# Kernel tuning notes

Hardware: AMD Instinct MI355X
Metric: run time of the kernel (lower is better)

Reference implementation:

```python
import jax, jax.numpy as jnp
import numpy as np

B, N, K = 8, 2048, 8
NEG_SLOPE = 0.2
EPS = 1e-5


def lrelu(x):
    return jax.nn.leaky_relu(x, NEG_SLOPE)


def bn(x, axes):
    # BatchNorm forward with batch statistics, affine at init (gamma=1, beta=0)
    m = x.mean(axes, keepdims=True)
    v = x.var(axes, keepdims=True)
    return (x - m) / jnp.sqrt(v + EPS)


def knn(x, k):
    # x: [B, C, N] -> idx [B, N, K] of nearest neighbors (incl. self), as in DGCNN
    xx = jnp.sum(x * x, axis=1)                      # [B, N]
    inner = jnp.einsum('bcn,bcm->bnm', x, x)         # [B, N, N]
    pair = -(xx[:, :, None] - 2.0 * inner + xx[:, None, :])  # -||xi-xj||^2
    return jax.lax.top_k(pair, k)[1]                 # [B, N, K]


def get_graph_feature(x, idx):
    # x: [B, C, N], idx: [B, N, K] -> [B, 2C, N, K] = cat(neighbor-center, center)
    nb = jax.vmap(lambda xb, ib: xb[:, ib])(x, idx)  # [B, C, N, K]
    ctr = x[:, :, :, None]
    return jnp.concatenate([nb - ctr, jnp.broadcast_to(ctr, nb.shape)], axis=1)


def edge_block(e, W):
    # 1x1 conv2d (no bias) + BN2d + LeakyReLU on [B, C, N, K]
    h = jnp.einsum('oc,bcnk->bonk', W, e)
    return lrelu(bn(h, (0, 2, 3)))


def setup_inputs() -> dict:
    key = jax.random.key(0)
    ks = jax.random.split(key, 10)
    def w(k, shape):
        fan_in = shape[-1]
        return jax.random.normal(k, shape, jnp.float32) / np.sqrt(fan_in)
    return {
        'x': jax.random.normal(ks[0], (B, N, 3), jnp.float32),
        'start_neighs': jax.random.randint(ks[1], (B, N, K), 0, N, jnp.int32),
        'u_noise': jax.random.uniform(ks[2], (B, 70, N), jnp.float32, 1e-6, 1.0 - 1e-6),
        'W0': w(ks[3], (64, 6)),
        'W1': w(ks[4], (128, 128)),
        'W2': w(ks[5], (256, 256)),
        'W3': w(ks[6], (512, 512)),
        'W4': w(ks[7], (1024, 960)),
        'Wm1': w(ks[8], (512, 1024)),
        'Wm2': w(ks[9], (70, 512)),
    }


def reference(x, start_neighs, u_noise, W0, W1, W2, W3, W4, Wm1, Wm2):
    xt = jnp.swapaxes(x, 1, 2)                        # [B, 3, N]
    # EdgeConv 0: uses provided start_neighs
    e = get_graph_feature(xt, start_neighs)           # [B, 6, N, K]
    h = edge_block(e, W0)                             # [B, 64, N, K]
    outs = [h.max(axis=-1)]                           # [B, 64, N]
    # EdgeConvs 1..3: dynamic knn on current features (only_true_neighs=False)
    for W in (W1, W2, W3):
        prev = outs[-1]
        idx = knn(prev, K)
        e = get_graph_feature(prev, idx)              # [B, 2C, N, K]
        h = edge_block(e, W)
        outs.append(h.max(axis=-1))
    cat = jnp.concatenate(outs, axis=1)               # [B, 960, N]
    feat = lrelu(bn(jnp.einsum('oc,bcn->bon', W4, cat), (0, 2)))  # [B, 1024, N]
    # masking prediction head
    hm = lrelu(bn(jnp.einsum('oc,bcn->bon', Wm1, feat), (0, 2)))  # [B, 512, N]
    logits = jnp.einsum('oc,bcn->bon', Wm2, hm)       # [B, 70, N]
    # gumbel softmax (tau=1, hard=True) over last dim (points), straight-through
    g = -jnp.log(-jnp.log(u_noise))
    soft = jax.nn.softmax(logits + g, axis=-1)
    hard = jax.nn.one_hot(jnp.argmax(soft, axis=-1), N, dtype=soft.dtype)
    y = hard + soft - jax.lax.stop_gradient(soft)     # values are exactly 0/1
    return jnp.transpose(y, (1, 0, 2))[..., None]     # [70, B, N, 1]
```

## Files before the change

### kernel.cpp

```cpp
#include <hip/hip_runtime.h>
#include <math.h>

#define Bsz 8
#define Nsz 2048
#define Ksz 8
#define NSLOPE 0.2f
#define EPSV 1e-5f
#define LOSCALE 2048.0f
#define INV_LOSCALE (1.0f / 2048.0f)

typedef _Float16 half8 __attribute__((ext_vector_type(8)));
typedef float floatx4 __attribute__((ext_vector_type(4)));

__device__ __forceinline__ int swzk(int k, int row)
{
    return (k & ~31) | ((((k >> 3) + (row >> 1)) & 3) << 3) | (k & 7);
}

__device__ __forceinline__ void glds16(const _Float16* g, _Float16* l)
{
    __builtin_amdgcn_global_load_lds(
        (const __attribute__((address_space(1))) unsigned int*)g,
        (__attribute__((address_space(3))) unsigned int*)l, 16, 0, 0);
}

__device__ __forceinline__ void split2(float v, _Float16& h, _Float16& l)
{
    _Float16 hh = (_Float16)v;
    h = hh;
    l = (_Float16)((v - (float)hh) * LOSCALE);
}

__device__ __forceinline__ unsigned long long shfl_xor64(unsigned long long x, int off)
{
    unsigned lo = __shfl_xor((unsigned)x, off, 64);
    unsigned hi = __shfl_xor((unsigned)(x >> 32), off, 64);
    return ((unsigned long long)hi << 32) | lo;
}

__device__ __forceinline__ void ins8_64(unsigned long long (&t)[8], unsigned long long key)
{
#pragma unroll
    for (int j = 7; j >= 1; --j)
        t[j] = (key > t[j - 1]) ? t[j - 1] : ((key > t[j]) ? key : t[j]);
    t[0] = (key > t[0]) ? key : t[0];
}

template <int EPI>
__launch_bounds__(512) __global__
void hgemm_k(const _Float16* __restrict__ Ahi, const _Float16* __restrict__ Alo,
             long long sAb, int lda,
             const _Float16* __restrict__ Bhi, const _Float16* __restrict__ Blo,
             long long sBb, int ldb,
             float* __restrict__ C, long long sCb, int ldc,
             int Mreal, int Kk, const float* __restrict__ xx)
{
    __shared__ _Float16 sm[16384];
    const int b = blockIdx.z;
    const int m0 = blockIdx.y * 128, n0 = blockIdx.x * 128;
    const int tid = threadIdx.x;
    const int w = tid >> 6, lane = tid & 63;
    const int quad = lane >> 4, r16 = lane & 15;
    const int wm = (w >> 1) * 32, wn = (w & 1) * 64;
    const int sq = (r16 >> 1) & 3;
    const int kchunk = ((quad + sq) & 3) * 8;

    const _Float16* Ah = Ahi + (long long)b * sAb;
    const _Float16* Al = Alo + (long long)b * sAb;
    const _Float16* Bh = Bhi + (long long)b * sBb;
    const _Float16* Bl = Blo + (long long)b * sBb;

    floatx4 acc_h[2][4], acc_m[2][4];
#pragma unroll
    for (int i = 0; i < 2; i++)
#pragma unroll
        for (int j = 0; j < 4; j++) {
            acc_h[i][j] = (floatx4){0.f, 0.f, 0.f, 0.f};
            acc_m[i][j] = (floatx4){0.f, 0.f, 0.f, 0.f};
        }

    const int srow = tid >> 2;
    const int sseg = (tid & 3) * 8;

    for (int k0 = 0; k0 < Kk; k0 += 32) {
        long long aoff = (long long)(m0 + srow) * lda + k0 + sseg;
        long long boff = (long long)(n0 + srow) * ldb + k0 + sseg;
        glds16(Ah + aoff, &sm[tid * 8]);
        glds16(Al + aoff, &sm[4096 + tid * 8]);
        glds16(Bh + boff, &sm[8192 + tid * 8]);
        glds16(Bl + boff, &sm[12288 + tid * 8]);
        __syncthreads();

        half8 ah[2], al[2];
#pragma unroll
        for (int i = 0; i < 2; i++) {
            int off = (wm + i * 16 + r16) * 32 + kchunk;
            ah[i] = *(const half8*)&sm[off];
            al[i] = *(const half8*)&sm[4096 + off];
        }
#pragma unroll
        for (int j = 0; j < 4; j++) {
            int off = (wn + j * 16 + r16) * 32 + kchunk;
            half8 bh = *(const half8*)&sm[8192 + off];
            half8 bl = *(const half8*)&sm[12288 + off];
#pragma unroll
            for (int i = 0; i < 2; i++) {
                acc_h[i][j] = __builtin_amdgcn_mfma_f32_16x16x32_f16(ah[i], bh, acc_h[i][j], 0, 0, 0);
                acc_m[i][j] = __builtin_amdgcn_mfma_f32_16x16x32_f16(ah[i], bl, acc_m[i][j], 0, 0, 0);
                acc_m[i][j] = __builtin_amdgcn_mfma_f32_16x16x32_f16(al[i], bh, acc_m[i][j], 0, 0, 0);
            }
        }
        __syncthreads();
    }

    float* Cb = C + (long long)b * sCb;
    const float* xxp = EPI ? (xx + (long long)b * Nsz) : xx;
#pragma unroll
    for (int i = 0; i < 2; i++) {
#pragma unroll
        for (int r = 0; r < 4; r++) {
            int gm = m0 + wm + i * 16 + quad * 4 + r;
            if (gm >= Mreal) continue;
            float xm = EPI ? xxp[gm] : 0.f;
#pragma unroll
            for (int j = 0; j < 4; j++) {
                int gn = n0 + wn + j * 16 + r16;
                float v = acc_h[i][j][r] + acc_m[i][j][r] * INV_LOSCALE;
                if (EPI == 1) v = -((xm - 2.f * v) + xxp[gn]);
                Cb[(long long)gm * ldc + gn] = v;
            }
        }
    }
}

__launch_bounds__(512) __global__
void hgemm_cand_k(const _Float16* __restrict__ Phi, const _Float16* __restrict__ Plo,
                  long long sPb, int ldp,
                  unsigned long long* __restrict__ cand,
                  int Kk, const float* __restrict__ xx)
{
    __shared__ float smf[64 * 129];
    _Float16* sm = (_Float16*)smf;
    const int b = blockIdx.z;
    const int m0 = blockIdx.y * 128, n0 = blockIdx.x * 128;
    const int tid = threadIdx.x;
    const int w = tid >> 6, lane = tid & 63;
    const int quad = lane >> 4, r16 = lane & 15;
    const int wm = (w >> 1) * 32, wn = (w & 1) * 64;
    const int sq = (r16 >> 1) & 3;
    const int kchunk = ((quad + sq) & 3) * 8;

    const _Float16* Ah = Phi + (long long)b * sPb;
    const _Float16* Al = Plo + (long long)b * sPb;

    floatx4 acc_h[2][4], acc_m[2][4];
#pragma unroll
    for (int i = 0; i < 2; i++)
#pragma unroll
        for (int j = 0; j < 4; j++) {
            acc_h[i][j] = (floatx4){0.f, 0.f, 0.f, 0.f};
            acc_m[i][j] = (floatx4){0.f, 0.f, 0.f, 0.f};
        }

    const int srow = tid >> 2;
    const int sseg = (tid & 3) * 8;

    for (int k0 = 0; k0 < Kk; k0 += 32) {
        long long aoff = (long long)(m0 + srow) * ldp + k0 + sseg;
        long long boff = (long long)(n0 + srow) * ldp + k0 + sseg;
        glds16(Ah + aoff, &sm[tid * 8]);
        glds16(Al + aoff, &sm[4096 + tid * 8]);
        glds16(Ah + boff, &sm[8192 + tid * 8]);
        glds16(Al + boff, &sm[12288 + tid * 8]);
        __syncthreads();

        half8 ah[2], al[2];
#pragma unroll
        for (int i = 0; i < 2; i++) {
            int off = (wm + i * 16 + r16) * 32 + kchunk;
            ah[i] = *(const half8*)&sm[off];
            al[i] = *(const half8*)&sm[4096 + off];
        }
#pragma unroll
        for (int j = 0; j < 4; j++) {
            int off = (wn + j * 16 + r16) * 32 + kchunk;
            half8 bh = *(const half8*)&sm[8192 + off];
            half8 bl = *(const half8*)&sm[12288 + off];
#pragma unroll
            for (int i = 0; i < 2; i++) {
                acc_h[i][j] = __builtin_amdgcn_mfma_f32_16x16x32_f16(ah[i], bh, acc_h[i][j], 0, 0, 0);
                acc_m[i][j] = __builtin_amdgcn_mfma_f32_16x16x32_f16(ah[i], bl, acc_m[i][j], 0, 0, 0);
                acc_m[i][j] = __builtin_amdgcn_mfma_f32_16x16x32_f16(al[i], bh, acc_m[i][j], 0, 0, 0);
            }
        }
        __syncthreads();
    }

    const float* xxp = xx + (long long)b * Nsz;
    const int row8 = tid >> 3;
    const int s8 = tid & 7;
    const int gshift = (lane >> 3) * 8;

#pragma unroll
    for (int p = 0; p < 2; p++) {
        __syncthreads();
        if ((w >> 2) == p) {
            int rbase = wm - p * 64;
#pragma unroll
            for (int i = 0; i < 2; i++) {
#pragma unroll
                for (int r = 0; r < 4; r++) {
                    int row_l = rbase + i * 16 + quad * 4 + r;
                    float xm = xxp[m0 + p * 64 + row_l];
#pragma unroll
                    for (int j = 0; j < 4; j++) {
                        int col = wn + j * 16 + r16;
                        float a = acc_h[i][j][r] + acc_m[i][j][r] * INV_LOSCALE;
                        smf[row_l * 129 + col] = -((xm - 2.f * a) + xxp[n0 + col]);
                    }
                }
            }
        }
        __syncthreads();

        unsigned vals[16];
#pragma unroll
        for (int c = 0; c < 16; c++) {
            unsigned u = __float_as_uint(smf[row8 * 129 + s8 + c * 8]);
            vals[c] = (u & 0x80000000u) ? ~u : (u | 0x80000000u);
        }
        unsigned t[8] = {0, 0, 0, 0, 0, 0, 0, 0};
#pragma unroll
        for (int c = 0; c < 16; c++) {
            unsigned key = vals[c];
#pragma unroll
            for (int j = 7; j >= 1; --j) {
                unsigned m = t[j - 1] < key ? t[j - 1] : key;
                t[j] = t[j] > m ? t[j] : m;
            }
            t[0] = t[0] > key ? t[0] : key;
        }
#pragma unroll
        for (int d = 1; d < 8; d <<= 1) {
            unsigned oth[8];
#pragma unroll
            for (int j = 0; j < 8; j++) oth[j] = __shfl_xor(t[j], d, 64);
            unsigned c2[8];
#pragma unroll
            for (int j = 0; j < 8; j++) {
                unsigned a = t[j], b2 = oth[7 - j];
                c2[j] = a > b2 ? a : b2;
            }
#define CE(A, B) { unsigned x = c2[A], y = c2[B]; c2[A] = x > y ? x : y; c2[B] = x > y ? y : x; }
            CE(0, 4) CE(1, 5) CE(2, 6) CE(3, 7)
            CE(0, 2) CE(1, 3) CE(4, 6) CE(5, 7)
            CE(0, 1) CE(2, 3) CE(4, 5) CE(6, 7)
#undef CE
#pragma unroll
            for (int j = 0; j < 8; j++) t[j] = c2[j];
        }
        const unsigned T = t[7];

        int gm = m0 + p * 64 + row8;
        unsigned long long* cp = cand + (((size_t)b * Nsz + gm) * 16 + blockIdx.x) * 8;
        const unsigned smask = (1u << s8) - 1u;
        int g = 0;
#pragma unroll
        for (int c = 0; c < 16; c++) {
            unsigned long long m = __ballot(vals[c] > T);
            unsigned byte = (unsigned)(m >> gshift) & 0xFFu;
            if (vals[c] > T) {
                int pos = g + __popc(byte & smask);
                int gn = n0 + s8 + c * 8;
                cp[pos] = ((unsigned long long)vals[c] << 32) | (0xFFFFFFFFu - (unsigned)gn);
            }
            g += __popc(byte);
        }
        const int needed = 8 - g;
        int e = 0;
        for (int c = 0; c < 16 && e < needed; c++) {
            unsigned long long m = __ballot(vals[c] == T);
            unsigned byte = (unsigned)(m >> gshift) & 0xFFu;
            int pos = e + __popc(byte & smask);
            if (vals[c] == T && pos < needed) {
                int gn = n0 + s8 + c * 8;
                cp[g + pos] = ((unsigned long long)T << 32) | (0xFFFFFFFFu - (unsigned)gn);
            }
            e += __popc(byte);
        }
    }
}

__global__ void merge_cand_k(const unsigned long long* __restrict__ cand,
                             int* __restrict__ idxo)
{
    int lane = threadIdx.x & 63;
    int row = blockIdx.x * 4 + (threadIdx.x >> 6);
    const unsigned long long* cr = cand + (size_t)row * 128;
    unsigned long long t[8] = {0, 0, 0, 0, 0, 0, 0, 0};
    ins8_64(t, cr[lane]);
    ins8_64(t, cr[lane + 64]);
    int* op = idxo + (size_t)row * 8;
#pragma unroll
    for (int r = 0; r < 8; r++) {
        unsigned long long best = t[0];
#pragma unroll
        for (int off = 32; off; off >>= 1) {
            unsigned long long o = shfl_xor64(best, off);
            if (o > best) best = o;
        }
        bool own = (t[0] == best);
#pragma unroll
        for (int j = 0; j < 7; j++) t[j] = own ? t[j + 1] : t[j];
        t[7] = own ? 0ull : t[7];
        if (lane == 0) op[r] = (int)(0xFFFFFFFFu - (unsigned)(best & 0xFFFFFFFFull));
    }
}

__launch_bounds__(256) __global__
void sgemm_k(const float* __restrict__ A, int lda,
             const float* __restrict__ Bm, long long sBb, int ldb,
             float* __restrict__ C, long long sCb, int ldc,
             int M, int Kk)
{
    __shared__ float As[16][64];
    __shared__ float Bs[16][64];
    const int b = blockIdx.z;
    const float* Bb = Bm + (long long)b * sBb;
    const int m0 = blockIdx.y * 64, n0 = blockIdx.x * 64;
    const int tid = threadIdx.x;
    const int am = tid >> 2, ak = (tid & 3) * 4;
    const int bk = tid >> 6, bn = tid & 63;
    const int tx = tid & 15, ty = tid >> 4;
    float acc[4][4] = {};
    for (int k0 = 0; k0 < Kk; k0 += 16) {
#pragma unroll
        for (int i = 0; i < 4; i++) {
            int gk = k0 + ak + i;
            int gm = m0 + am;
            As[ak + i][am] = (gk < Kk && gm < M) ? A[(long long)gm * lda + gk] : 0.f;
        }
#pragma unroll
        for (int i = 0; i < 4; i++) {
            int kk = bk + i * 4;
            int gk = k0 + kk;
            Bs[kk][bn] = (gk < Kk) ? Bb[(long long)gk * ldb + (n0 + bn)] : 0.f;
        }
        __syncthreads();
#pragma unroll
        for (int kk = 0; kk < 16; kk++) {
            float a[4], bb2[4];
#pragma unroll
            for (int i = 0; i < 4; i++) a[i] = As[kk][ty * 4 + i];
#pragma unroll
            for (int j = 0; j < 4; j++) bb2[j] = Bs[kk][tx * 4 + j];
#pragma unroll
            for (int i = 0; i < 4; i++)
#pragma unroll
                for (int j = 0; j < 4; j++)
                    acc[i][j] = fmaf(a[i], bb2[j], acc[i][j]);
        }
        __syncthreads();
    }
    float* Cb = C + (long long)b * sCb;
#pragma unroll
    for (int i = 0; i < 4; i++) {
        int gm = m0 + ty * 4 + i;
        if (gm >= M) continue;
#pragma unroll
        for (int j = 0; j < 4; j++)
            Cb[(long long)gm * ldc + n0 + tx * 4 + j] = acc[i][j];
    }
}

#define T0 16384
#define T1 (T0 + 192)
#define T2 (T1 + 16384)
#define T3 (T2 + 65536)
#define T4 (T3 + 262144)
#define T5 (T4 + 983040)
#define T6 (T5 + 524288)
#define T7 (T6 + 65536)
#define WOFF_E1 0
#define WOFF_E2 16384
#define WOFF_E3 81920
#define WOFF_W4 344064
#define WOFF_M1 1327104
#define WOFF_M2 1851392

__device__ __forceinline__ void split_plain(const float* W, _Float16* wh, _Float16* wl,
                                            size_t base, int t, int M, int Kk)
{
    int oo = t / Kk, c = t - oo * Kk;
    float v = (oo < M) ? W[(size_t)oo * Kk + c] : 0.f;
    _Float16 h, l;
    split2(v, h, l);
    size_t d = base + (size_t)oo * Kk + swzk(c, oo);
    wh[d] = h; wl[d] = l;
}

__device__ __forceinline__ void split_edge(const float* W, _Float16* wh, _Float16* wl,
                                           size_t base, int t, int O, int C)
{
    int oo = t / C, c = t - oo * C;
    float v;
    if (oo < O) v = W[(size_t)oo * 2 * C + c];
    else { int o2 = oo - O; v = W[(size_t)o2 * 2 * C + C + c] - W[(size_t)o2 * 2 * C + c]; }
    _Float16 h, l;
    split2(v, h, l);
    size_t d = base + (size_t)oo * C + swzk(c, oo);
    wh[d] = h; wl[d] = l;
}

__global__ void mega_prep_k(const float* __restrict__ x,
                            const float* __restrict__ W0, const float* __restrict__ W1,
                            const float* __restrict__ W2, const float* __restrict__ W3,
                            const float* __restrict__ W4, const float* __restrict__ Wm1,
                            const float* __restrict__ Wm2,
                            float* __restrict__ xt, float* __restrict__ wcat32,
                            _Float16* __restrict__ wh, _Float16* __restrict__ wl)
{
    int t = blockIdx.x * 256 + threadIdx.x;
    if (t < T0) {
        int n = t & (Nsz - 1), b = t >> 11;
#pragma unroll
        for (int c = 0; c < 3; c++)
            xt[((size_t)b * 3 + c) * Nsz + n] = x[((size_t)b * Nsz + n) * 3 + c];
    } else if (t < T1) {
        int u = t - T0;
        int oo = u / 3, c = u % 3;
        float a = W0[(size_t)oo * 6 + c];
        float b2 = W0[(size_t)oo * 6 + 3 + c];
        wcat32[(size_t)oo * 3 + c] = a;
        wcat32[(size_t)(64 + oo) * 3 + c] = b2 - a;
    } else if (t < T2) {
        split_edge(W1, wh, wl, WOFF_E1, t - T1, 128, 64);
    } else if (t < T3) {
        split_edge(W2, wh, wl, WOFF_E2, t - T2, 256, 128);
    } else if (t < T4) {
        split_edge(W3, wh, wl, WOFF_E3, t - T3, 512, 256);
    } else if (t < T5) {
        split_plain(W4, wh, wl, WOFF_W4, t - T4, 1024, 960);
    } else if (t < T6) {
        split_plain(Wm1, wh, wl, WOFF_M1, t - T5, 512, 1024);
    } else if (t < T7) {
        split_plain(Wm2, wh, wl, WOFF_M2, t - T6, 70, 512);
    }
}

__global__ void xx_planes_k(const _Float16* __restrict__ catA, const _Float16* __restrict__ catB,
                            float* __restrict__ xx, int off, int C)
{
    int t = blockIdx.x * 256 + threadIdx.x;
    if (t >= Bsz * Nsz) return;
    int n = t & (Nsz - 1), b = t >> 11;
    size_t base = ((size_t)b * Nsz + n) * 1024 + off;
    float s = 0.f;
    for (int c8 = 0; c8 < C / 8; c8++) {
        half8 h = *(const half8*)&catA[base + c8 * 8];
        half8 l = *(const half8*)&catB[base + c8 * 8];
#pragma unroll
        for (int e = 0; e < 8; e++) {
            float vh = (float)h[e];
            float vl = (float)l[e] * INV_LOSCALE;
            s = fmaf(vh, vh, s);
            s = fmaf(2.f * vh, vl, s);
        }
    }
    xx[t] = s;
}

__global__ void gather_pool_t_k(const float* __restrict__ R, const int* __restrict__ idx,
                                _Float16* __restrict__ catA, _Float16* __restrict__ catB,
                                float* __restrict__ part, int O, int off)
{
    __shared__ float tile[64][65];
    const int tid = threadIdx.x;
    const int lane = tid & 63, w = tid >> 6;
    const int n0 = blockIdx.x * 64, o0 = blockIdx.y * 64, b = blockIdx.z;
    const int n = n0 + lane;

    int id[8];
    {
        const int* ip = idx + ((size_t)b * Nsz + n) * 8;
#pragma unroll
        for (int k = 0; k < 8; k++) id[k] = ip[k];
    }
    const float* Rb = R + (size_t)b * 2 * O * Nsz;
#pragma unroll
    for (int i = 0; i < 16; i++) {
        int o_l = w + i * 4;
        int o = o0 + o_l;
        const float* P = Rb + (size_t)o * Nsz;
        float q = Rb[(size_t)(O + o) * Nsz + n];
        float hmax = -INFINITY, s1 = 0.f, s2 = 0.f;
#pragma unroll
        for (int k = 0; k < 8; k++) {
            float h = P[id[k]] + q;
            hmax = fmaxf(hmax, h);
            s1 += h;
            s2 += h * h;
        }
        tile[o_l][lane] = hmax;
#pragma unroll
        for (int offs = 32; offs; offs >>= 1) {
            s1 += __shfl_xor(s1, offs, 64);
            s2 += __shfl_xor(s2, offs, 64);
        }
        if (lane == 0) {
            size_t pi = ((size_t)o * Bsz + b) * 32 + blockIdx.x;
            part[pi * 2] = s1;
            part[pi * 2 + 1] = s2;
        }
    }
    __syncthreads();
    int n_l = tid >> 2, quad = tid & 3;
    int nrow = n0 + n_l;
    half8 h0, h1, l0, l1;
#pragma unroll
    for (int e = 0; e < 8; e++) {
        _Float16 hh, ll;
        split2(tile[quad * 16 + e][n_l], hh, ll);
        h0[e] = hh; l0[e] = ll;
        split2(tile[quad * 16 + 8 + e][n_l], hh, ll);
        h1[e] = hh; l1[e] = ll;
    }
    size_t rowb = ((size_t)b * Nsz + nrow) * 1024;
    int c0 = off + o0 + quad * 16;
    *(half8*)&catA[rowb + swzk(c0, nrow)] = h0;
    *(half8*)&catA[rowb + swzk(c0 + 8, nrow)] = h1;
    *(half8*)&catB[rowb + swzk(c0, nrow)] = l0;
    *(half8*)&catB[rowb + swzk(c0 + 8, nrow)] = l1;
}

__global__ void stats_reduce_k(const float* __restrict__ part, float* __restrict__ stats)
{
    int o2 = blockIdx.x;
    int t = threadIdx.x;
    float s1 = part[((size_t)o2 * 256 + t) * 2];
    float s2 = part[((size_t)o2 * 256 + t) * 2 + 1];
#pragma unroll
    for (int off = 32; off; off >>= 1) { s1 += __shfl_xor(s1, off, 64); s2 += __shfl_xor(s2, off, 64); }
    __shared__ float sh[8];
    int w = t >> 6;
    if ((t & 63) == 0) { sh[w] = s1; sh[4 + w] = s2; }
    __syncthreads();
    if (t == 0) {
        stats[2 * o2] = sh[0] + sh[1] + sh[2] + sh[3];
        stats[2 * o2 + 1] = sh[4] + sh[5] + sh[6] + sh[7];
    }
}

__global__ void fc_stats_k(const float* __restrict__ buf, float* __restrict__ stats, int O)
{
    int oo = blockIdx.x;
    int t = threadIdx.x;
    float s1 = 0.f, s2 = 0.f;
    for (int i = t; i < Bsz * Nsz; i += 256) {
        int b = i >> 11, n = i & (Nsz - 1);
        float v = buf[((size_t)b * O + oo) * Nsz + n];
        s1 += v; s2 += v * v;
    }
#pragma unroll
    for (int off = 32; off; off >>= 1) { s1 += __shfl_xor(s1, off, 64); s2 += __shfl_xor(s2, off, 64); }
    __shared__ float sh[8];
    int w = t >> 6;
    if ((t & 63) == 0) { sh[w] = s1; sh[4 + w] = s2; }
    __syncthreads();
    if (t == 0) {
        stats[2 * oo] = sh[0] + sh[1] + sh[2] + sh[3];
        stats[2 * oo + 1] = sh[4] + sh[5] + sh[6] + sh[7];
    }
}

__global__ void bn_t_k(_Float16* __restrict__ catA, _Float16* __restrict__ catB,
                       const float* __restrict__ stats, int off, int O, float invCnt)
{
    int per_n = O / 8;
    size_t t = (size_t)blockIdx.x * 256 + threadIdx.x;
    if (t >= (size_t)Bsz * Nsz * per_n) return;
    int c8 = (int)(t % per_n);
    size_t rest = t / per_n;
    int n = (int)(rest & (Nsz - 1));
    int b = (int)(rest >> 11);
    size_t base = ((size_t)b * Nsz + n) * 1024 + off + c8 * 8;
    int oo_base = ((c8 >> 2) << 5) + ((((c8 & 3) - (n >> 1)) & 3) << 3);
    half8 h = *(const half8*)&catA[base];
    half8 l = *(const half8*)&catB[base];
    half8 ho, lo;
#pragma unroll
    for (int e = 0; e < 8; e++) {
        int oo = oo_base + e;
        float mean = stats[2 * oo] * invCnt;
        float var = stats[2 * oo + 1] * invCnt - mean * mean;
        float v = (float)h[e] + (float)l[e] * INV_LOSCALE;
        float z = (v - mean) / sqrtf(var + EPSV);
        z = z >= 0.f ? z : NSLOPE * z;
        _Float16 hh, ll;
        split2(z, hh, ll);
        ho[e] = hh; lo[e] = ll;
    }
    *(half8*)&catA[base] = ho;
    *(half8*)&catB[base] = lo;
}

__global__ void bn_split_t_k(const float* __restrict__ src, const float* __restrict__ stats,
                             _Float16* __restrict__ dA, _Float16* __restrict__ dB,
                             int O, int ldt, float invCnt)
{
    __shared__ float tile[64][65];
    const int tid = threadIdx.x;
    const int n0 = blockIdx.x * 64, o0 = blockIdx.y * 64, b = blockIdx.z;
#pragma unroll
    for (int i = 0; i < 16; i++) {
        int flat = tid + 256 * i;
        int o_l = flat >> 6, n_l = flat & 63;
        int oo = o0 + o_l;
        float mean = stats[2 * oo] * invCnt;
        float var = stats[2 * oo + 1] * invCnt - mean * mean;
        float v = src[((size_t)b * O + oo) * Nsz + n0 + n_l];
        float z = (v - mean) / sqrtf(var + EPSV);
        tile[o_l][n_l] = z >= 0.f ? z : NSLOPE * z;
    }
    __syncthreads();
    int n_l = tid >> 2, quad = tid & 3;
    int nrow = n0 + n_l;
    half8 h0, h1, l0, l1;
#pragma unroll
    for (int e = 0; e < 8; e++) {
        _Float16 hh, ll;
        split2(tile[quad * 16 + e][n_l], hh, ll);
        h0[e] = hh; l0[e] = ll;
        split2(tile[quad * 16 + 8 + e][n_l], hh, ll);
        h1[e] = hh; l1[e] = ll;
    }
    size_t rowb = ((size_t)b * Nsz + nrow) * ldt;
    int c0 = o0 + quad * 16;
    *(half8*)&dA[rowb + swzk(c0, nrow)] = h0;
    *(half8*)&dA[rowb + swzk(c0 + 8, nrow)] = h1;
    *(half8*)&dB[rowb + swzk(c0, nrow)] = l0;
    *(half8*)&dB[rowb + swzk(c0 + 8, nrow)] = l1;
}

__global__ void gumbel_onehot_k(const float* __restrict__ logits, const float* __restrict__ u,
                                float* __restrict__ out)
{
    int lane = threadIdx.x & 63;
    int wv = threadIdx.x >> 6;
    int row = blockIdx.x * 4 + wv;
    int b = row / 70, oo = row % 70;
    const float* L = logits + (size_t)row * Nsz;
    const float* U = u + (size_t)row * Nsz;
    float bv = -INFINITY; int bi = 0x7fffffff;
    for (int n = lane; n < Nsz; n += 64) {
        float g = -logf(-logf(U[n]));
        float z = L[n] + g;
        if (z > bv) { bv = z; bi = n; }
    }
#pragma unroll
    for (int off = 32; off; off >>= 1) {
        float ov = __shfl_xor(bv, off, 64);
        int oi = __shfl_xor(bi, off, 64);
        if (ov > bv || (ov == bv && oi < bi)) { bv = ov; bi = oi; }
    }
    float* Or = out + ((size_t)oo * Bsz + b) * Nsz;
    for (int n = lane; n < Nsz; n += 64) Or[n] = (n == bi) ? 1.f : 0.f;
}

extern "C" void kernel_launch(void* const* d_in, const int* in_sizes, int n_in,
                              void* d_out, int out_size, void* d_ws, size_t ws_size,
                              hipStream_t stream)
{
    (void)in_sizes; (void)n_in; (void)out_size; (void)ws_size;
    const float* x   = (const float*)d_in[0];
    const int*   sn  = (const int*)d_in[1];
    const float* un  = (const float*)d_in[2];
    const float* W0  = (const float*)d_in[3];
    const float* W1  = (const float*)d_in[4];
    const float* W2  = (const float*)d_in[5];
    const float* W3  = (const float*)d_in[6];
    const float* W4  = (const float*)d_in[7];
    const float* Wm1 = (const float*)d_in[8];
    const float* Wm2 = (const float*)d_in[9];
    float* out = (float*)d_out;

    char* ws = (char*)d_ws;
    size_t o = 0;
    _Float16* catA = (_Float16*)(ws + o); o += (size_t)Bsz * Nsz * 1024 * 2;
    _Float16* catB = (_Float16*)(ws + o); o += (size_t)Bsz * Nsz * 1024 * 2;
    float* R       = (float*)(ws + o);    o += (size_t)Bsz * 1024 * Nsz * 4;
    _Float16* wHi  = (_Float16*)(ws + o); o += (size_t)2 * 1024 * 1024 * 2;
    _Float16* wLo  = (_Float16*)(ws + o); o += (size_t)2 * 1024 * 1024 * 2;
    float* xt      = (float*)(ws + o);    o += (size_t)Bsz * 3 * Nsz * 4;
    float* xxb     = (float*)(ws + o);    o += (size_t)Bsz * Nsz * 4;
    float* wcat32  = (float*)(ws + o);    o += 4096;
    float* part    = (float*)(ws + o);    o += (size_t)512 * Bsz * 32 * 2 * 4;
    float* stats   = (float*)(ws + o);    o += 2048 * 4;
    int* idxb      = (int*)(ws + o);      o += (size_t)Bsz * Nsz * Ksz * 4;
    unsigned long long* cand = (unsigned long long*)R;
    float* logits  = R + (size_t)12 * 1024 * 1024;

    const long long catStride = (long long)Nsz * 1024;

    mega_prep_k<<<(T7 + 255) / 256, 256, 0, stream>>>(x, W0, W1, W2, W3, W4, Wm1, Wm2,
                                                      xt, wcat32, wHi, wLo);

    sgemm_k<<<dim3(32, 2, Bsz), 256, 0, stream>>>(wcat32, 3, xt, 3LL * Nsz, Nsz,
                                                  R, 2LL * 64 * Nsz, Nsz, 128, 3);
    gather_pool_t_k<<<dim3(32, 1, Bsz), 256, 0, stream>>>(R, sn, catA, catB, part, 64, 0);
    stats_reduce_k<<<64, 256, 0, stream>>>(part, stats);
    bn_t_k<<<(int)(((size_t)Bsz * Nsz * 8 + 255) / 256), 256, 0, stream>>>(
        catA, catB, stats, 0, 64, 1.f / 131072.f);

    struct LayerDesc { int C; int O; int prevOff; int catOff; size_t woff; };
    LayerDesc L[3] = {
        { 64, 128, 0, 64, WOFF_E1 },
        { 128, 256, 64, 192, WOFF_E2 },
        { 256, 512, 192, 448, WOFF_E3 },
    };
    for (int li = 0; li < 3; li++) {
        int C = L[li].C, O = L[li].O;
        int poff = L[li].prevOff;
        xx_planes_k<<<(Bsz * Nsz + 255) / 256, 256, 0, stream>>>(catA, catB, xxb, poff, C);
        hgemm_cand_k<<<dim3(16, 16, Bsz), 512, 0, stream>>>(
            catA + poff, catB + poff, catStride, 1024, cand, C, xxb);
        merge_cand_k<<<Bsz * Nsz / 4, 256, 0, stream>>>(cand, idxb);
        hgemm_k<0><<<dim3(16, 2 * O / 128, Bsz), 512, 0, stream>>>(
            wHi + L[li].woff, wLo + L[li].woff, 0, C, catA + poff, catB + poff, catStride, 1024,
            R, 2LL * O * Nsz, Nsz, 2 * O, C, nullptr);
        gather_pool_t_k<<<dim3(32, O / 64, Bsz), 256, 0, stream>>>(
            R, idxb, catA, catB, part, O, L[li].catOff);
        stats_reduce_k<<<O, 256, 0, stream>>>(part, stats);
        bn_t_k<<<(int)(((size_t)Bsz * Nsz * (O / 8) + 255) / 256), 256, 0, stream>>>(
            catA, catB, stats, L[li].catOff, O, 1.f / 131072.f);
    }

    hgemm_k<0><<<dim3(16, 8, Bsz), 512, 0, stream>>>(
        wHi + WOFF_W4, wLo + WOFF_W4, 0, 960, catA, catB, catStride, 1024,
        R, 1024LL * Nsz, Nsz, 1024, 960, nullptr);
    fc_stats_k<<<1024, 256, 0, stream>>>(R, stats, 1024);
    bn_split_t_k<<<dim3(32, 16, Bsz), 256, 0, stream>>>(R, stats, catA, catB, 1024, 1024,
                                                        1.f / 16384.f);
    hgemm_k<0><<<dim3(16, 4, Bsz), 512, 0, stream>>>(
        wHi + WOFF_M1, wLo + WOFF_M1, 0, 1024, catA, catB, catStride, 1024,
        R, 512LL * Nsz, Nsz, 512, 1024, nullptr);
    fc_stats_k<<<512, 256, 0, stream>>>(R, stats, 512);
    bn_split_t_k<<<dim3(32, 8, Bsz), 256, 0, stream>>>(R, stats, catA, catB, 512, 512,
                                                       1.f / 16384.f);
    hgemm_k<0><<<dim3(16, 1, Bsz), 512, 0, stream>>>(
        wHi + WOFF_M2, wLo + WOFF_M2, 0, 512, catA, catB, (long long)Nsz * 512, 512,
        logits, 70LL * Nsz, Nsz, 70, 512, nullptr);

    gumbel_onehot_k<<<(Bsz * 70) / 4, 256, 0, stream>>>(logits, un, out);
}
```

Measured before the change: 955.6 us.

## Compute symmetric pairwise-distance tiles once and materialize full matrix for row top-k

Replaces the fused GEMM+candidate-extraction kNN path with a GEMM that computes only upper-triangular tiles of the symmetric distance matrix. Each off-diagonal tile is also written transposed, so the full matrix is stored in global memory. A separate per-row top-8 threshold kernel then scans full rows. The batch is processed in two chunks of 4 so the N×N matrix fits in the workspace. This roughly halves the MFMA work but adds a large write and re-read of the distance matrix (4×2048×2048 floats per chunk), in exchange for removing the candidate buffer and merge pass.

```diff
diff --git a/kernel.cpp b/kernel.cpp
--- a/kernel.cpp
+++ b/kernel.cpp
@@ -29,21 +29,6 @@
     _Float16 hh = (_Float16)v;
     h = hh;
     l = (_Float16)((v - (float)hh) * LOSCALE);
-}
-
-__device__ __forceinline__ unsigned long long shfl_xor64(unsigned long long x, int off)
-{
-    unsigned lo = __shfl_xor((unsigned)x, off, 64);
-    unsigned hi = __shfl_xor((unsigned)(x >> 32), off, 64);
-    return ((unsigned long long)hi << 32) | lo;
-}
-
-__device__ __forceinline__ void ins8_64(unsigned long long (&t)[8], unsigned long long key)
-{
-#pragma unroll
-    for (int j = 7; j >= 1; --j)
-        t[j] = (key > t[j - 1]) ? t[j - 1] : ((key > t[j]) ? key : t[j]);
-    t[0] = (key > t[0]) ? key : t[0];
 }
 
 template <int EPI>
@@ -134,15 +119,20 @@
 }
 
 __launch_bounds__(512) __global__
-void hgemm_cand_k(const _Float16* __restrict__ Phi, const _Float16* __restrict__ Plo,
-                  long long sPb, int ldp,
-                  unsigned long long* __restrict__ cand,
-                  int Kk, const float* __restrict__ xx)
+void hgemm_sym_k(const _Float16* __restrict__ Phi, const _Float16* __restrict__ Plo,
+                 long long sPb, int ldp,
+                 float* __restrict__ C, long long sCb, int ldc,
+                 int Kk, const float* __restrict__ xx)
 {
     __shared__ float smf[64 * 129];
     _Float16* sm = (_Float16*)smf;
     const int b = blockIdx.z;
-    const int m0 = blockIdx.y * 128, n0 = blockIdx.x * 128;
+    int bx = blockIdx.x;
+    int ti = 0;
+    while (bx >= 16 - ti) { bx -= 16 - ti; ti++; }
+    const int tj = ti + bx;
+    const int m0 = ti * 128, n0 = tj * 128;
+
     const int tid = threadIdx.x;
     const int w = tid >> 6, lane = tid & 63;
     const int quad = lane >> 4, r16 = lane & 15;
@@ -196,10 +186,24 @@
         __syncthreads();
     }
 
+    float* Cb = C + (long long)b * sCb;
     const float* xxp = xx + (long long)b * Nsz;
-    const int row8 = tid >> 3;
-    const int s8 = tid & 7;
-    const int gshift = (lane >> 3) * 8;
+
+#pragma unroll
+    for (int i = 0; i < 2; i++) {
+#pragma unroll
+        for (int r = 0; r < 4; r++) {
+            int gm = m0 + wm + i * 16 + quad * 4 + r;
+            float xm = xxp[gm];
+#pragma unroll
+            for (int j = 0; j < 4; j++) {
+                int gn = n0 + wn + j * 16 + r16;
+                float v = acc_h[i][j][r] + acc_m[i][j][r] * INV_LOSCALE;
+                Cb[(long long)gm * ldc + gn] = -((xm - 2.f * v) + xxp[gn]);
+            }
+        }
+    }
+    if (ti == tj) return;
 
 #pragma unroll
     for (int p = 0; p < 2; p++) {
@@ -215,105 +219,91 @@
 #pragma unroll
                     for (int j = 0; j < 4; j++) {
                         int col = wn + j * 16 + r16;
-                        float a = acc_h[i][j][r] + acc_m[i][j][r] * INV_LOSCALE;
-                        smf[row_l * 129 + col] = -((xm - 2.f * a) + xxp[n0 + col]);
+                        float v = acc_h[i][j][r] + acc_m[i][j][r] * INV_LOSCALE;
+                        smf[row_l * 129 + col] = -((xm - 2.f * v) + xxp[n0 + col]);
                     }
                 }
             }
         }
         __syncthreads();
-
-        unsigned vals[16];
-#pragma unroll
-        for (int c = 0; c < 16; c++) {
-            unsigned u = __float_as_uint(smf[row8 * 129 + s8 + c * 8]);
-            vals[c] = (u & 0x80000000u) ? ~u : (u | 0x80000000u);
-        }
-        unsigned t[8] = {0, 0, 0, 0, 0, 0, 0, 0};
-#pragma unroll
-        for (int c = 0; c < 16; c++) {
-            unsigned key = vals[c];
-#pragma unroll
-            for (int j = 7; j >= 1; --j) {
-                unsigned m = t[j - 1] < key ? t[j - 1] : key;
-                t[j] = t[j] > m ? t[j] : m;
-            }
-            t[0] = t[0] > key ? t[0] : key;
-        }
-#pragma unroll
-        for (int d = 1; d < 8; d <<= 1) {
-            unsigned oth[8];
-#pragma unroll
-            for (int j = 0; j < 8; j++) oth[j] = __shfl_xor(t[j], d, 64);
-            unsigned c2[8];
-#pragma unroll
-            for (int j = 0; j < 8; j++) {
-                unsigned a = t[j], b2 = oth[7 - j];
-                c2[j] = a > b2 ? a : b2;
-            }
+        int mr = tid >> 2;
+        int e0 = (tid & 3) * 16;
+        float* dst = Cb + (long long)(n0 + mr) * ldc + m0 + p * 64 + e0;
+#pragma unroll
+        for (int e4 = 0; e4 < 4; e4++) {
+            float4 v4;
+            v4.x = smf[(e0 + e4 * 4 + 0) * 129 + mr];
+            v4.y = smf[(e0 + e4 * 4 + 1) * 129 + mr];
+            v4.z = smf[(e0 + e4 * 4 + 2) * 129 + mr];
+            v4.w = smf[(e0 + e4 * 4 + 3) * 129 + mr];
+            *(float4*)&dst[e4 * 4] = v4;
+        }
+    }
+}
+
+__launch_bounds__(256) __global__
+void topk8_thresh_k(const float* __restrict__ pair, int* __restrict__ idxo)
+{
+    const int lane = threadIdx.x & 63;
+    const int row = blockIdx.x * 4 + (threadIdx.x >> 6);
+    const float* pr = pair + (size_t)row * Nsz;
+
+    unsigned vals[32];
+#pragma unroll
+    for (int c = 0; c < 32; c++) {
+        unsigned u = __float_as_uint(pr[c * 64 + lane]);
+        vals[c] = (u & 0x80000000u) ? ~u : (u | 0x80000000u);
+    }
+
+    unsigned t[8] = {0, 0, 0, 0, 0, 0, 0, 0};
+#pragma unroll
+    for (int c = 0; c < 32; c++) {
+        unsigned key = vals[c];
+#pragma unroll
+        for (int j = 7; j >= 1; --j) {
+            unsigned m = t[j - 1] < key ? t[j - 1] : key;
+            t[j] = t[j] > m ? t[j] : m;
+        }
+        t[0] = t[0] > key ? t[0] : key;
+    }
+#pragma unroll
+    for (int d = 1; d < 64; d <<= 1) {
+        unsigned oth[8];
+#pragma unroll
+        for (int j = 0; j < 8; j++) oth[j] = __shfl_xor(t[j], d, 64);
+        unsigned c2[8];
+#pragma unroll
+        for (int j = 0; j < 8; j++) {
+            unsigned a = t[j], b2 = oth[7 - j];
+            c2[j] = a > b2 ? a : b2;
+        }
 #define CE(A, B) { unsigned x = c2[A], y = c2[B]; c2[A] = x > y ? x : y; c2[B] = x > y ? y : x; }
-            CE(0, 4) CE(1, 5) CE(2, 6) CE(3, 7)
-            CE(0, 2) CE(1, 3) CE(4, 6) CE(5, 7)
-            CE(0, 1) CE(2, 3) CE(4, 5) CE(6, 7)
+        CE(0, 4) CE(1, 5) CE(2, 6) CE(3, 7)
+        CE(0, 2) CE(1, 3) CE(4, 6) CE(5, 7)
+        CE(0, 1) CE(2, 3) CE(4, 5) CE(6, 7)
 #undef CE
 #pragma unroll
-            for (int j = 0; j < 8; j++) t[j] = c2[j];
-        }
-        const unsigned T = t[7];
-
-        int gm = m0 + p * 64 + row8;
-        unsigned long long* cp = cand + (((size_t)b * Nsz + gm) * 16 + blockIdx.x) * 8;
-        const unsigned smask = (1u << s8) - 1u;
-        int g = 0;
-#pragma unroll
-        for (int c = 0; c < 16; c++) {
-            unsigned long long m = __ballot(vals[c] > T);
-            unsigned byte = (unsigned)(m >> gshift) & 0xFFu;
-            if (vals[c] > T) {
-                int pos = g + __popc(byte & smask);
-                int gn = n0 + s8 + c * 8;
-                cp[pos] = ((unsigned long long)vals[c] << 32) | (0xFFFFFFFFu - (unsigned)gn);
-            }
-            g += __popc(byte);
-        }
-        const int needed = 8 - g;
-        int e = 0;
-        for (int c = 0; c < 16 && e < needed; c++) {
-            unsigned long long m = __ballot(vals[c] == T);
-            unsigned byte = (unsigned)(m >> gshift) & 0xFFu;
-            int pos = e + __popc(byte & smask);
-            if (vals[c] == T && pos < needed) {
-                int gn = n0 + s8 + c * 8;
-                cp[g + pos] = ((unsigned long long)T << 32) | (0xFFFFFFFFu - (unsigned)gn);
-            }
-            e += __popc(byte);
-        }
-    }
-}
-
-__global__ void merge_cand_k(const unsigned long long* __restrict__ cand,
-                             int* __restrict__ idxo)
-{
-    int lane = threadIdx.x & 63;
-    int row = blockIdx.x * 4 + (threadIdx.x >> 6);
-    const unsigned long long* cr = cand + (size_t)row * 128;
-    unsigned long long t[8] = {0, 0, 0, 0, 0, 0, 0, 0};
-    ins8_64(t, cr[lane]);
-    ins8_64(t, cr[lane + 64]);
+        for (int j = 0; j < 8; j++) t[j] = c2[j];
+    }
+    const unsigned T = t[7];
+
+    const unsigned long long lmask = (1ull << lane) - 1ull;
     int* op = idxo + (size_t)row * 8;
-#pragma unroll
-    for (int r = 0; r < 8; r++) {
-        unsigned long long best = t[0];
-#pragma unroll
-        for (int off = 32; off; off >>= 1) {
-            unsigned long long o = shfl_xor64(best, off);
-            if (o > best) best = o;
-        }
-        bool own = (t[0] == best);
-#pragma unroll
-        for (int j = 0; j < 7; j++) t[j] = own ? t[j + 1] : t[j];
-        t[7] = own ? 0ull : t[7];
-        if (lane == 0) op[r] = (int)(0xFFFFFFFFu - (unsigned)(best & 0xFFFFFFFFull));
+    int g = 0;
+#pragma unroll
+    for (int c = 0; c < 32; c++) {
+        unsigned long long m = __ballot(vals[c] > T);
+        if (vals[c] > T) op[g + __popcll(m & lmask)] = c * 64 + lane;
+        g += __popcll(m);
+    }
+    const int needed = 8 - g;
+    int e = 0;
+    for (int c = 0; c < 32; c++) {
+        if (e >= needed) break;
+        unsigned long long m = __ballot(vals[c] == T);
+        int pos = e + __popcll(m & lmask);
+        if (vals[c] == T && pos < needed) op[g + pos] = c * 64 + lane;
+        e += __popcll(m);
     }
 }
 
@@ -697,7 +687,6 @@
     float* part    = (float*)(ws + o);    o += (size_t)512 * Bsz * 32 * 2 * 4;
     float* stats   = (float*)(ws + o);    o += 2048 * 4;
     int* idxb      = (int*)(ws + o);      o += (size_t)Bsz * Nsz * Ksz * 4;
-    unsigned long long* cand = (unsigned long long*)R;
     float* logits  = R + (size_t)12 * 1024 * 1024;
 
     const long long catStride = (long long)Nsz * 1024;
@@ -722,9 +711,14 @@
         int C = L[li].C, O = L[li].O;
         int poff = L[li].prevOff;
         xx_planes_k<<<(Bsz * Nsz + 255) / 256, 256, 0, stream>>>(catA, catB, xxb, poff, C);
-        hgemm_cand_k<<<dim3(16, 16, Bsz), 512, 0, stream>>>(
-            catA + poff, catB + poff, catStride, 1024, cand, C, xxb);
-        merge_cand_k<<<Bsz * Nsz / 4, 256, 0, stream>>>(cand, idxb);
+        for (int ch = 0; ch < 2; ch++) {
+            const _Float16* pA = catA + poff + (size_t)ch * 4 * catStride;
+            const _Float16* pB = catB + poff + (size_t)ch * 4 * catStride;
+            hgemm_sym_k<<<dim3(136, 1, 4), 512, 0, stream>>>(
+                pA, pB, catStride, 1024,
+                R, (long long)Nsz * Nsz, Nsz, C, xxb + (size_t)ch * 4 * Nsz);
+            topk8_thresh_k<<<4 * Nsz / 4, 256, 0, stream>>>(R, idxb + (size_t)ch * 4 * Nsz * Ksz);
+        }
         hgemm_k<0><<<dim3(16, 2 * O / 128, Bsz), 512, 0, stream>>>(
             wHi + L[li].woff, wLo + L[li].woff, 0, C, catA + poff, catB + poff, catStride, 1024,
             R, 2LL * O * Nsz, Nsz, 2 * O, C, nullptr);
```

Result: no change. 958.5 us (+0.3%).
